# Kernel tuning notes

Hardware: AMD Instinct MI355X
Metric: run time of the kernel (lower is better)

## Reference

```python
import jax, jax.numpy as jnp
import numpy as np

B, S, H = 4, 1024, 1024
NH, HD = 16, 64  # num heads, head dim


def setup_inputs() -> dict:
    key = jax.random.key(0)
    ks = jax.random.split(key, 7)
    scale = 1.0 / np.sqrt(H)
    return {
        "hidden_states": jax.random.normal(ks[0], (B, S, H), jnp.float32),
        "attention_mask": jnp.zeros((B, 1, 1, S), jnp.float32),
        "Wq": jax.random.normal(ks[1], (H, H), jnp.float32) * scale,
        "bq": jnp.zeros((H,), jnp.float32),
        "Wk": jax.random.normal(ks[2], (H, H), jnp.float32) * scale,
        "bk": jnp.zeros((H,), jnp.float32),
        "Wv": jax.random.normal(ks[3], (H, H), jnp.float32) * scale,
        "bv": jnp.zeros((H,), jnp.float32),
    }


def _heads(x):
    # [B,S,H] -> [B,NH,S,HD]
    return x.reshape(x.shape[0], x.shape[1], NH, HD).transpose(0, 2, 1, 3)


def reference(hidden_states, attention_mask, Wq, bq, Wk, bk, Wv, bv):
    q = _heads(hidden_states @ Wq + bq)  # [B,NH,S,HD]
    k = _heads(hidden_states @ Wk + bk)
    v = _heads(hidden_states @ Wv + bv)
    scores = jnp.einsum("bhqd,bhkd->bhqk", q, k) / np.sqrt(HD)
    scores = scores + attention_mask  # broadcast additive mask
    probs = jax.nn.softmax(scores, axis=-1)  # dropout p=0 (eval)
    ctx = jnp.einsum("bhqk,bhkd->bhqd", probs, v)
    # [B,NH,S,HD] -> [B,S,H]
    return ctx.transpose(0, 2, 1, 3).reshape(hidden_states.shape[0], hidden_states.shape[1], NH * HD)
```

## Files before the change

### kernel.cpp

```cpp
#include <hip/hip_runtime.h>
#include <hip/hip_bf16.h>

typedef __bf16 bf16_t;
typedef __bf16 bf16x8 __attribute__((ext_vector_type(8)));
typedef float f32x4 __attribute__((ext_vector_type(4)));
typedef float f32x16 __attribute__((ext_vector_type(16)));
typedef unsigned uint2v __attribute__((ext_vector_type(2)));

#define MFMA16(a, b, c) __builtin_amdgcn_mfma_f32_16x16x32_bf16((a), (b), (c), 0, 0, 0)
#define MFMA32(a, b, c) __builtin_amdgcn_mfma_f32_32x32x16_bf16((a), (b), (c), 0, 0, 0)

static constexpr int BB = 4, SS = 1024, HH = 1024, NHEAD = 16, HDIM = 64;
static constexpr int MM = BB * SS;

__device__ __forceinline__ void gload_lds16(const void* g, void* l) {
  __builtin_amdgcn_global_load_lds((const __attribute__((address_space(1))) void*)g,
                                   (__attribute__((address_space(3))) void*)l, 16, 0, 0);
}

#if __has_builtin(__builtin_amdgcn_permlane32_swap)
#define PSWAP(a, b)                                                    \
  {                                                                    \
    uint2v _r = __builtin_amdgcn_permlane32_swap((a), (b), false, false); \
    (a) = _r.x;                                                        \
    (b) = _r.y;                                                        \
  }
#else
#define PSWAP(a, b) asm("v_permlane32_swap_b32 %0, %1" : "+v"(a), "+v"(b))
#endif

#if __has_builtin(__builtin_amdgcn_exp2f)
__device__ __forceinline__ float EXP2(float x) { return __builtin_amdgcn_exp2f(x); }
#else
__device__ __forceinline__ float EXP2(float x) {
  float r;
  asm("v_exp_f32 %0, %1" : "=v"(r) : "v"(x));
  return r;
}
#endif

__global__ __launch_bounds__(256) void cvt_bf16_kernel(const float* __restrict__ in,
                                                       bf16_t* __restrict__ out, int n) {
  int i = (blockIdx.x * 256 + threadIdx.x) * 8;
  if (i >= n) return;
  float4 a = *(const float4*)(in + i);
  float4 b = *(const float4*)(in + i + 4);
  union { int4 i4; bf16_t h[8]; } u;
  u.h[0] = (bf16_t)a.x; u.h[1] = (bf16_t)a.y; u.h[2] = (bf16_t)a.z; u.h[3] = (bf16_t)a.w;
  u.h[4] = (bf16_t)b.x; u.h[5] = (bf16_t)b.y; u.h[6] = (bf16_t)b.z; u.h[7] = (bf16_t)b.w;
  *(int4*)(out + i) = u.i4;
}

__global__ __launch_bounds__(256) void transposeW_kernel(const float* __restrict__ Wq,
                                                         const float* __restrict__ Wk,
                                                         const float* __restrict__ Wv,
                                                         bf16_t* __restrict__ WT) {
  __shared__ float tile[32][33];
  int z = blockIdx.z;
  const float* W = (z == 0) ? Wq : (z == 1) ? Wk : Wv;
  bf16_t* Out = WT + (size_t)z * HH * HH;
  int tx = threadIdx.x, ty = threadIdx.y;
  int x0 = blockIdx.x * 32;
  int y0 = blockIdx.y * 32;
  for (int j = ty; j < 32; j += 8)
    tile[j][tx] = W[(size_t)(y0 + j) * HH + x0 + tx];
  __syncthreads();
  for (int j = ty; j < 32; j += 8)
    Out[(size_t)(x0 + j) * HH + y0 + tx] = (bf16_t)tile[tx][j];
}

#define BMT 128
#define BNT 384
#define BKT 64
#define NTL 16
#define BUFBYTES 65536

__global__ __launch_bounds__(512, 2) void qkv_gemm2(const bf16_t* __restrict__ hiddenB,
                                                    const bf16_t* __restrict__ WT,
                                                    const float* __restrict__ bq,
                                                    const float* __restrict__ bk,
                                                    const float* __restrict__ bv,
                                                    bf16_t* __restrict__ Qo,
                                                    bf16_t* __restrict__ Ko,
                                                    bf16_t* __restrict__ Vt) {
  __shared__ bf16_t smem[2 * BUFBYTES / 2];

  const int wg = blockIdx.x;
  const int id = (wg & 7) * 32 + (wg >> 3);
  const int nb = id & 7;
  const int mb = id >> 3;

  const int t = threadIdx.x;
  const int lane = t & 63;
  const int w = t >> 6;
  const int wr = w >> 2;
  const int wc = w & 3;
  const int lr = lane & 15;
  const int g4 = lane >> 4;

  const unsigned schunk = (((unsigned)(t & 7)) ^ ((unsigned)((t >> 3) & 7))) << 4;
  const char* Ag = (const char*)hiddenB + (size_t)(mb * BMT) * 2048;
  const char* Bg = (const char*)WT + (size_t)(nb * BNT) * 2048;

  auto stage = [&](const char* gb, int growbase, int kbyte, char* ldsdest) {
    gload_lds16(gb + (size_t)(growbase + (t >> 3)) * 2048 + kbyte + schunk,
                ldsdest + w * 1024);
  };
  const unsigned axor = ((unsigned)(lr & 7)) << 4;

  f32x4 acc[4][6] = {};

  {
    char* S0 = (char*)smem;
    stage(Ag, 0, 0, S0);
    stage(Ag, 64, 0, S0 + 8192);
#pragma unroll
    for (int i = 0; i < 6; ++i) stage(Bg, i * 64, 0, S0 + 16384 + i * 8192);
  }
  asm volatile("s_waitcnt vmcnt(0)" ::: "memory");
  __builtin_amdgcn_s_barrier();

  for (int j = 0; j < NTL; ++j) {
    const char* Ab = (const char*)smem + (j & 1) * BUFBYTES;
    const char* Bb = Ab + 16384;
    char* Sb = (char*)smem + ((j + 1) & 1) * BUFBYTES;
    const int kb = (j + 1) * 128;
    const bool st = (j + 1 < NTL);

    if (st) { stage(Ag, 0, kb, Sb); stage(Ag, 64, kb, Sb + 8192); }

    bf16x8 af[4][2];
#pragma unroll
    for (int mi = 0; mi < 4; ++mi)
#pragma unroll
      for (int ks = 0; ks < 2; ++ks)
        af[mi][ks] = *(const bf16x8*)(Ab + (size_t)(wr * 64 + mi * 16 + lr) * 128 +
                                      (((unsigned)(ks * 64 + g4 * 16)) ^ axor));

#pragma unroll
    for (int p = 0; p < 3; ++p) {
      if (st) {
        stage(Bg, (2 * p) * 64, kb, Sb + 16384 + (2 * p) * 8192);
        stage(Bg, (2 * p + 1) * 64, kb, Sb + 16384 + (2 * p + 1) * 8192);
      }
      bf16x8 b0[2], b1[2];
#pragma unroll
      for (int ks = 0; ks < 2; ++ks) {
        b0[ks] = *(const bf16x8*)(Bb + (size_t)(wc * 96 + (2 * p) * 16 + lr) * 128 +
                                  (((unsigned)(ks * 64 + g4 * 16)) ^ axor));
        b1[ks] = *(const bf16x8*)(Bb + (size_t)(wc * 96 + (2 * p + 1) * 16 + lr) * 128 +
                                  (((unsigned)(ks * 64 + g4 * 16)) ^ axor));
      }
      __builtin_amdgcn_s_setprio(1);
#pragma unroll
      for (int mi = 0; mi < 4; ++mi)
#pragma unroll
        for (int ks = 0; ks < 2; ++ks) {
          acc[mi][2 * p] = MFMA16(af[mi][ks], b0[ks], acc[mi][2 * p]);
          acc[mi][2 * p + 1] = MFMA16(af[mi][ks], b1[ks], acc[mi][2 * p + 1]);
        }
      __builtin_amdgcn_s_setprio(0);
    }

    if (st) {
      asm volatile("s_waitcnt vmcnt(0)" ::: "memory");
      __builtin_amdgcn_s_barrier();
    }
  }

#pragma unroll
  for (int ni = 0; ni < 6; ++ni) {
    int col = nb * BNT + wc * 96 + ni * 16 + lr;
    int z = col >> 10;
    int ci = col & 1023;
    const float* bias = (z == 0) ? bq : (z == 1) ? bk : bv;
    float bia = bias[ci];
    int hh = ci >> 6, d = ci & 63;
    if (z < 2) {
      bf16_t* Out = (z == 0) ? Qo : Ko;
#pragma unroll
      for (int mi = 0; mi < 4; ++mi) {
#pragma unroll
        for (int r = 0; r < 4; ++r) {
          int row = mb * BMT + wr * 64 + mi * 16 + g4 * 4 + r;
          int b = row >> 10, s = row & 1023;
          Out[((size_t)(b * NHEAD + hh) * SS + s) * HDIM + d] = (bf16_t)(acc[mi][ni][r] + bia);
        }
      }
    } else {
#pragma unroll
      for (int mi = 0; mi < 4; ++mi) {
        int row0 = mb * BMT + wr * 64 + mi * 16 + g4 * 4;
        int b = row0 >> 10, s0 = row0 & 1023;
        float v0 = acc[mi][ni][0] + bia, v1 = acc[mi][ni][1] + bia;
        float v2 = acc[mi][ni][2] + bia, v3 = acc[mi][ni][3] + bia;
        unsigned u0, u1;
        asm("v_cvt_pk_bf16_f32 %0, %1, %2" : "=v"(u0) : "v"(v0), "v"(v1));
        asm("v_cvt_pk_bf16_f32 %0, %1, %2" : "=v"(u1) : "v"(v2), "v"(v3));
        uint2 pv; pv.x = u0; pv.y = u1;
        *(uint2*)&Vt[((size_t)(b * NHEAD + hh) * HDIM + d) * SS + s0] = pv;
      }
    }
  }
}

__global__ __launch_bounds__(256) void attn5_kernel(const bf16_t* __restrict__ Q,
                                                    const bf16_t* __restrict__ K,
                                                    const bf16_t* __restrict__ Vt,
                                                    const float* __restrict__ mask,
                                                    float* __restrict__ out) {
  __shared__ bf16_t KVsm[3][2][64 * 64];
  __shared__ float Msm[SS];

  const int wg = blockIdx.x;
  const int id = (wg & 7) * 64 + (wg >> 3);
  const int xblk = id & 7;
  const int bh = id >> 3;

  const int b = bh >> 4;
  const int h = bh & 15;
  const int t = threadIdx.x;
  const int lane = t & 63;
  const int w = t >> 6;
  const int l31 = lane & 31;
  const int hi = lane >> 5;
  const int q0 = xblk * 128 + w * 32;

  const bf16_t* Qh = Q + (size_t)bh * SS * HDIM;
  const bf16_t* Kh = K + (size_t)bh * SS * HDIM;
  const bf16_t* Vh = Vt + (size_t)bh * HDIM * SS;

  const float L2E = 1.4426950408889634f;
  {
    float4 mv = *(const float4*)&mask[(size_t)b * SS + t * 4];
    mv.x *= L2E; mv.y *= L2E; mv.z *= L2E; mv.w *= L2E;
    *(float4*)&Msm[t * 4] = mv;
  }

  bf16x8 qb[4];
#pragma unroll
  for (int c = 0; c < 4; ++c) {
    bf16x8 q = *(const bf16x8*)&Qh[(size_t)(q0 + l31) * HDIM + c * 16 + hi * 8];
#pragma unroll
    for (int e = 0; e < 8; ++e) q[e] = (bf16_t)((float)q[e] * (0.125f * L2E));
    qb[c] = q;
  }

  const int srow = lane >> 3;
  const unsigned gcol = ((lane & 7) * 16) ^ (srow << 4);
  const unsigned swz = (unsigned)((l31 & 7) << 4);

  auto stageKV = [&](int tile, int buf) {
    const int kv0 = tile * 64;
#pragma unroll
    for (int i = 0; i < 2; ++i) {
      int rbase = w * 16 + i * 8;
      gload_lds16((const char*)Kh + (size_t)(kv0 + rbase + srow) * 128 + gcol,
                  (char*)&KVsm[buf][0][0] + (size_t)rbase * 128);
      gload_lds16((const char*)Vh + (size_t)(rbase + srow) * 2048 + (size_t)kv0 * 2 + gcol,
                  (char*)&KVsm[buf][1][0] + (size_t)rbase * 128);
    }
  };

  f32x16 acc0 = {}, acc1 = {};
  float m_run = -1e30f, l_run = 0.f;

  stageKV(0, 0);
  stageKV(1, 1);
  asm volatile("s_waitcnt vmcnt(4) lgkmcnt(0)" ::: "memory");
  __builtin_amdgcn_s_barrier();

  for (int tt = 0; tt < 16; ++tt) {
    if (tt + 2 < 16) stageKV(tt + 2, (tt + 2) % 3);
    const char* Kb = (const char*)&KVsm[tt % 3][0][0];
    const char* Vb = (const char*)&KVsm[tt % 3][1][0];
    const int kv0 = tt * 64;

    f32x16 st0 = {}, st1 = {};
    __builtin_amdgcn_s_setprio(1);
#pragma unroll
    for (int c = 0; c < 4; ++c) {
      bf16x8 kf0 = *(const bf16x8*)(Kb + (size_t)l31 * 128 + ((unsigned)(c * 32 + hi * 16) ^ swz));
      st0 = MFMA32(kf0, qb[c], st0);
    }
#pragma unroll
    for (int c = 0; c < 4; ++c) {
      bf16x8 kf1 = *(const bf16x8*)(Kb + (size_t)(32 + l31) * 128 + ((unsigned)(c * 32 + hi * 16) ^ swz));
      st1 = MFMA32(kf1, qb[c], st1);
    }
    __builtin_amdgcn_s_setprio(0);

#pragma unroll
    for (int k2 = 0; k2 < 8; ++k2) {
      int off = 8 * (k2 >> 1) + 4 * hi + 2 * (k2 & 1);
      float2 m0v = *(const float2*)&Msm[kv0 + off];
      float2 m1v = *(const float2*)&Msm[kv0 + 32 + off];
      st0[2 * k2] += m0v.x; st0[2 * k2 + 1] += m0v.y;
      st1[2 * k2] += m1v.x; st1[2 * k2 + 1] += m1v.y;
    }

    float v0 = fmaxf(st0[0], st1[0]),  v1 = fmaxf(st0[1], st1[1]);
    float v2 = fmaxf(st0[2], st1[2]),  v3 = fmaxf(st0[3], st1[3]);
    float v4 = fmaxf(st0[4], st1[4]),  v5 = fmaxf(st0[5], st1[5]);
    float v6 = fmaxf(st0[6], st1[6]),  v7 = fmaxf(st0[7], st1[7]);
    float v8 = fmaxf(st0[8], st1[8]),  v9 = fmaxf(st0[9], st1[9]);
    float v10 = fmaxf(st0[10], st1[10]), v11 = fmaxf(st0[11], st1[11]);
    float v12 = fmaxf(st0[12], st1[12]), v13 = fmaxf(st0[13], st1[13]);
    float v14 = fmaxf(st0[14], st1[14]), v15 = fmaxf(st0[15], st1[15]);
    float g0 = fmaxf(fmaxf(v0, v1), v2);
    float g1 = fmaxf(fmaxf(v3, v4), v5);
    float g2 = fmaxf(fmaxf(v6, v7), v8);
    float g3 = fmaxf(fmaxf(v9, v10), v11);
    float g4 = fmaxf(fmaxf(v12, v13), v14);
    float mj = fmaxf(fmaxf(fmaxf(g0, g1), g2), fmaxf(fmaxf(g3, g4), v15));
    mj = fmaxf(mj, __shfl_xor(mj, 32));

    if (!__all(mj <= m_run + 8.f)) {
      float mnew = fmaxf(m_run, mj);
      float corr = EXP2(m_run - mnew);
#pragma unroll
      for (int r = 0; r < 16; ++r) { acc0[r] *= corr; acc1[r] *= corr; }
      l_run *= corr;
      m_run = mnew;
    }

#pragma unroll
    for (int r = 0; r < 16; ++r) st0[r] = EXP2(st0[r] - m_run);
#pragma unroll
    for (int r = 0; r < 16; ++r) st1[r] = EXP2(st1[r] - m_run);

    float s0 = (st0[0] + st1[0]) + (st0[1] + st1[1]);
    float s1 = (st0[2] + st1[2]) + (st0[3] + st1[3]);
    float s2 = (st0[4] + st1[4]) + (st0[5] + st1[5]);
    float s3 = (st0[6] + st1[6]) + (st0[7] + st1[7]);
    float s4 = (st0[8] + st1[8]) + (st0[9] + st1[9]);
    float s5 = (st0[10] + st1[10]) + (st0[11] + st1[11]);
    float s6 = (st0[12] + st1[12]) + (st0[13] + st1[13]);
    float s7 = (st0[14] + st1[14]) + (st0[15] + st1[15]);
    float ls = ((s0 + s1) + (s2 + s3)) + ((s4 + s5) + (s6 + s7));
    ls += __shfl_xor(ls, 32);
    l_run += ls;

    unsigned wd0[8], wd1[8];
#pragma unroll
    for (int k2 = 0; k2 < 8; ++k2) {
      unsigned r0, r1;
      float a0f = st0[2 * k2], a1f = st0[2 * k2 + 1];
      float b0f = st1[2 * k2], b1f = st1[2 * k2 + 1];
      asm("v_cvt_pk_bf16_f32 %0, %1, %2" : "=v"(r0) : "v"(a0f), "v"(a1f));
      asm("v_cvt_pk_bf16_f32 %0, %1, %2" : "=v"(r1) : "v"(b0f), "v"(b1f));
      wd0[k2] = r0; wd1[k2] = r1;
    }
    unsigned a0 = wd0[0], b0 = wd0[2]; PSWAP(a0, b0);
    unsigned a1 = wd0[1], b1 = wd0[3]; PSWAP(a1, b1);
    unsigned a2 = wd0[4], b2 = wd0[6]; PSWAP(a2, b2);
    unsigned a3 = wd0[5], b3 = wd0[7]; PSWAP(a3, b3);
    unsigned c0 = wd1[0], d0 = wd1[2]; PSWAP(c0, d0);
    unsigned c1 = wd1[1], d1 = wd1[3]; PSWAP(c1, d1);
    unsigned c2 = wd1[4], d2 = wd1[6]; PSWAP(c2, d2);
    unsigned c3 = wd1[5], d3 = wd1[7]; PSWAP(c3, d3);
    union { unsigned u[4]; bf16x8 v; } pf0, pf1, pf2, pf3;
    pf0.u[0] = a0; pf0.u[1] = a1; pf0.u[2] = b0; pf0.u[3] = b1;
    pf1.u[0] = a2; pf1.u[1] = a3; pf1.u[2] = b2; pf1.u[3] = b3;
    pf2.u[0] = c0; pf2.u[1] = c1; pf2.u[2] = d0; pf2.u[3] = d1;
    pf3.u[0] = c2; pf3.u[1] = c3; pf3.u[2] = d2; pf3.u[3] = d3;

    __builtin_amdgcn_s_setprio(1);
    {
      bf16x8 vf;
      vf = *(const bf16x8*)(Vb + (size_t)(0 * 32 + l31) * 128 + ((unsigned)(0 * 64 + 0 * 32 + hi * 16) ^ swz));
      acc0 = MFMA32(vf, pf0.v, acc0);
      vf = *(const bf16x8*)(Vb + (size_t)(1 * 32 + l31) * 128 + ((unsigned)(0 * 64 + 0 * 32 + hi * 16) ^ swz));
      acc1 = MFMA32(vf, pf0.v, acc1);
      vf = *(const bf16x8*)(Vb + (size_t)(0 * 32 + l31) * 128 + ((unsigned)(0 * 64 + 1 * 32 + hi * 16) ^ swz));
      acc0 = MFMA32(vf, pf1.v, acc0);
      vf = *(const bf16x8*)(Vb + (size_t)(1 * 32 + l31) * 128 + ((unsigned)(0 * 64 + 1 * 32 + hi * 16) ^ swz));
      acc1 = MFMA32(vf, pf1.v, acc1);
      vf = *(const bf16x8*)(Vb + (size_t)(0 * 32 + l31) * 128 + ((unsigned)(1 * 64 + 0 * 32 + hi * 16) ^ swz));
      acc0 = MFMA32(vf, pf2.v, acc0);
      vf = *(const bf16x8*)(Vb + (size_t)(1 * 32 + l31) * 128 + ((unsigned)(1 * 64 + 0 * 32 + hi * 16) ^ swz));
      acc1 = MFMA32(vf, pf2.v, acc1);
      vf = *(const bf16x8*)(Vb + (size_t)(0 * 32 + l31) * 128 + ((unsigned)(1 * 64 + 1 * 32 + hi * 16) ^ swz));
      acc0 = MFMA32(vf, pf3.v, acc0);
      vf = *(const bf16x8*)(Vb + (size_t)(1 * 32 + l31) * 128 + ((unsigned)(1 * 64 + 1 * 32 + hi * 16) ^ swz));
      acc1 = MFMA32(vf, pf3.v, acc1);
    }
    __builtin_amdgcn_s_setprio(0);

    if (tt < 14) {
      asm volatile("s_waitcnt vmcnt(4)" ::: "memory");
      __builtin_amdgcn_s_barrier();
    } else if (tt == 14) {
      asm volatile("s_waitcnt vmcnt(0)" ::: "memory");
      __builtin_amdgcn_s_barrier();
    }
  }

  float rinv = 1.0f / l_run;
  int q = q0 + l31;
  float* ob = out + ((size_t)(b * SS + q)) * HH + h * HDIM;
#pragma unroll
  for (int g = 0; g < 4; ++g) {
    float4 o0, o1;
    o0.x = acc0[g * 4 + 0] * rinv; o0.y = acc0[g * 4 + 1] * rinv;
    o0.z = acc0[g * 4 + 2] * rinv; o0.w = acc0[g * 4 + 3] * rinv;
    o1.x = acc1[g * 4 + 0] * rinv; o1.y = acc1[g * 4 + 1] * rinv;
    o1.z = acc1[g * 4 + 2] * rinv; o1.w = acc1[g * 4 + 3] * rinv;
    *(float4*)&ob[g * 8 + 4 * hi] = o0;
    *(float4*)&ob[32 + g * 8 + 4 * hi] = o1;
  }
}

extern "C" void kernel_launch(void* const* d_in, const int* in_sizes, int n_in,
                              void* d_out, int out_size, void* d_ws, size_t ws_size,
                              hipStream_t stream) {
  const float* hs   = (const float*)d_in[0];
  const float* mask = (const float*)d_in[1];
  const float* Wq   = (const float*)d_in[2];
  const float* bq   = (const float*)d_in[3];
  const float* Wk   = (const float*)d_in[4];
  const float* bk   = (const float*)d_in[5];
  const float* Wv   = (const float*)d_in[6];
  const float* bv   = (const float*)d_in[7];
  float* out = (float*)d_out;

  char* ws = (char*)d_ws;
  bf16_t* hiddenB = (bf16_t*)ws;
  bf16_t* WT      = (bf16_t*)(ws + (size_t)8 * 1024 * 1024);
  bf16_t* Qb      = (bf16_t*)(ws + (size_t)14 * 1024 * 1024);
  bf16_t* Kb      = (bf16_t*)(ws + (size_t)22 * 1024 * 1024);
  bf16_t* Vt      = (bf16_t*)(ws + (size_t)30 * 1024 * 1024);

  cvt_bf16_kernel<<<MM * HH / (256 * 8), 256, 0, stream>>>(hs, hiddenB, MM * HH);
  transposeW_kernel<<<dim3(32, 32, 3), dim3(32, 8), 0, stream>>>(Wq, Wk, Wv, WT);
  qkv_gemm2<<<256, 512, 0, stream>>>(hiddenB, WT, bq, bk, bv, Qb, Kb, Vt);
  attn5_kernel<<<512, 256, 0, stream>>>(Qb, Kb, Vt, mask, out);
}
```

Baseline: 78.70 us.

## Split attention KV range across two wave groups with LDS merge of partial softmax

The attention kernel now launches 512 threads per block. Two groups of four waves each process half of the key/value sequence with double buffering, where before four waves streamed a triple-buffered pipeline over the full sequence. The second half writes its partial accumulators and running max/sum into LDS, and the first half rescales and merges them before writing output. This doubles the waves available to hide latency, but adds a merge step and uses a shallower prefetch with a full vmcnt(0) wait every iteration.

```diff
diff --git a/kernel.cpp b/kernel.cpp
--- a/kernel.cpp
+++ b/kernel.cpp
@@ -29,15 +29,11 @@
 #define PSWAP(a, b) asm("v_permlane32_swap_b32 %0, %1" : "+v"(a), "+v"(b))
 #endif
 
-#if __has_builtin(__builtin_amdgcn_exp2f)
-__device__ __forceinline__ float EXP2(float x) { return __builtin_amdgcn_exp2f(x); }
-#else
 __device__ __forceinline__ float EXP2(float x) {
   float r;
   asm("v_exp_f32 %0, %1" : "=v"(r) : "v"(x));
   return r;
 }
-#endif
 
 __global__ __launch_bounds__(256) void cvt_bf16_kernel(const float* __restrict__ in,
                                                        bf16_t* __restrict__ out, int n) {
@@ -204,12 +200,12 @@
   }
 }
 
-__global__ __launch_bounds__(256) void attn5_kernel(const bf16_t* __restrict__ Q,
-                                                    const bf16_t* __restrict__ K,
-                                                    const bf16_t* __restrict__ Vt,
-                                                    const float* __restrict__ mask,
-                                                    float* __restrict__ out) {
-  __shared__ bf16_t KVsm[3][2][64 * 64];
+__global__ __launch_bounds__(512, 4) void attn6_kernel(const bf16_t* __restrict__ Q,
+                                                       const bf16_t* __restrict__ K,
+                                                       const bf16_t* __restrict__ Vt,
+                                                       const float* __restrict__ mask,
+                                                       float* __restrict__ out) {
+  __shared__ bf16_t KVsm[2][2][2][64 * 64];
   __shared__ float Msm[SS];
 
   const int wg = blockIdx.x;
@@ -222,16 +218,19 @@
   const int t = threadIdx.x;
   const int lane = t & 63;
   const int w = t >> 6;
+  const int wl = w & 3;
+  const int half = w >> 2;
   const int l31 = lane & 31;
   const int hi = lane >> 5;
-  const int q0 = xblk * 128 + w * 32;
+  const int q0 = xblk * 128 + wl * 32;
+  const int kvbase = half * 512;
 
   const bf16_t* Qh = Q + (size_t)bh * SS * HDIM;
   const bf16_t* Kh = K + (size_t)bh * SS * HDIM;
   const bf16_t* Vh = Vt + (size_t)bh * HDIM * SS;
 
   const float L2E = 1.4426950408889634f;
-  {
+  if (t < 256) {
     float4 mv = *(const float4*)&mask[(size_t)b * SS + t * 4];
     mv.x *= L2E; mv.y *= L2E; mv.z *= L2E; mv.w *= L2E;
     *(float4*)&Msm[t * 4] = mv;
@@ -251,14 +250,14 @@
   const unsigned swz = (unsigned)((l31 & 7) << 4);
 
   auto stageKV = [&](int tile, int buf) {
-    const int kv0 = tile * 64;
+    const int kv0 = kvbase + tile * 64;
 #pragma unroll
     for (int i = 0; i < 2; ++i) {
-      int rbase = w * 16 + i * 8;
+      int rbase = wl * 16 + i * 8;
       gload_lds16((const char*)Kh + (size_t)(kv0 + rbase + srow) * 128 + gcol,
-                  (char*)&KVsm[buf][0][0] + (size_t)rbase * 128);
+                  (char*)&KVsm[half][buf][0][0] + (size_t)rbase * 128);
       gload_lds16((const char*)Vh + (size_t)(rbase + srow) * 2048 + (size_t)kv0 * 2 + gcol,
-                  (char*)&KVsm[buf][1][0] + (size_t)rbase * 128);
+                  (char*)&KVsm[half][buf][1][0] + (size_t)rbase * 128);
     }
   };
 
@@ -266,15 +265,14 @@
   float m_run = -1e30f, l_run = 0.f;
 
   stageKV(0, 0);
-  stageKV(1, 1);
-  asm volatile("s_waitcnt vmcnt(4) lgkmcnt(0)" ::: "memory");
+  asm volatile("s_waitcnt vmcnt(0)" ::: "memory");
   __builtin_amdgcn_s_barrier();
 
-  for (int tt = 0; tt < 16; ++tt) {
-    if (tt + 2 < 16) stageKV(tt + 2, (tt + 2) % 3);
-    const char* Kb = (const char*)&KVsm[tt % 3][0][0];
-    const char* Vb = (const char*)&KVsm[tt % 3][1][0];
-    const int kv0 = tt * 64;
+  for (int tt = 0; tt < 8; ++tt) {
+    if (tt + 1 < 8) stageKV(tt + 1, (tt + 1) & 1);
+    const char* Kb = (const char*)&KVsm[half][tt & 1][0][0];
+    const char* Vb = (const char*)&KVsm[half][tt & 1][1][0];
+    const int kv0 = kvbase + tt * 64;
 
     f32x16 st0 = {}, st1 = {};
     __builtin_amdgcn_s_setprio(1);
@@ -368,46 +366,69 @@
     __builtin_amdgcn_s_setprio(1);
     {
       bf16x8 vf;
-      vf = *(const bf16x8*)(Vb + (size_t)(0 * 32 + l31) * 128 + ((unsigned)(0 * 64 + 0 * 32 + hi * 16) ^ swz));
+      vf = *(const bf16x8*)(Vb + (size_t)(l31) * 128 + ((unsigned)(0 * 32 + hi * 16) ^ swz));
       acc0 = MFMA32(vf, pf0.v, acc0);
-      vf = *(const bf16x8*)(Vb + (size_t)(1 * 32 + l31) * 128 + ((unsigned)(0 * 64 + 0 * 32 + hi * 16) ^ swz));
+      vf = *(const bf16x8*)(Vb + (size_t)(32 + l31) * 128 + ((unsigned)(0 * 32 + hi * 16) ^ swz));
       acc1 = MFMA32(vf, pf0.v, acc1);
-      vf = *(const bf16x8*)(Vb + (size_t)(0 * 32 + l31) * 128 + ((unsigned)(0 * 64 + 1 * 32 + hi * 16) ^ swz));
+      vf = *(const bf16x8*)(Vb + (size_t)(l31) * 128 + ((unsigned)(1 * 32 + hi * 16) ^ swz));
       acc0 = MFMA32(vf, pf1.v, acc0);
-      vf = *(const bf16x8*)(Vb + (size_t)(1 * 32 + l31) * 128 + ((unsigned)(0 * 64 + 1 * 32 + hi * 16) ^ swz));
+      vf = *(const bf16x8*)(Vb + (size_t)(32 + l31) * 128 + ((unsigned)(1 * 32 + hi * 16) ^ swz));
       acc1 = MFMA32(vf, pf1.v, acc1);
-      vf = *(const bf16x8*)(Vb + (size_t)(0 * 32 + l31) * 128 + ((unsigned)(1 * 64 + 0 * 32 + hi * 16) ^ swz));
+      vf = *(const bf16x8*)(Vb + (size_t)(l31) * 128 + ((unsigned)(2 * 32 + hi * 16) ^ swz));
       acc0 = MFMA32(vf, pf2.v, acc0);
-      vf = *(const bf16x8*)(Vb + (size_t)(1 * 32 + l31) * 128 + ((unsigned)(1 * 64 + 0 * 32 + hi * 16) ^ swz));
+      vf = *(const bf16x8*)(Vb + (size_t)(32 + l31) * 128 + ((unsigned)(2 * 32 + hi * 16) ^ swz));
       acc1 = MFMA32(vf, pf2.v, acc1);
-      vf = *(const bf16x8*)(Vb + (size_t)(0 * 32 + l31) * 128 + ((unsigned)(1 * 64 + 1 * 32 + hi * 16) ^ swz));
+      vf = *(const bf16x8*)(Vb + (size_t)(l31) * 128 + ((unsigned)(3 * 32 + hi * 16) ^ swz));
       acc0 = MFMA32(vf, pf3.v, acc0);
-      vf = *(const bf16x8*)(Vb + (size_t)(1 * 32 + l31) * 128 + ((unsigned)(1 * 64 + 1 * 32 + hi * 16) ^ swz));
+      vf = *(const bf16x8*)(Vb + (size_t)(32 + l31) * 128 + ((unsigned)(3 * 32 + hi * 16) ^ swz));
       acc1 = MFMA32(vf, pf3.v, acc1);
     }
     __builtin_amdgcn_s_setprio(0);
 
-    if (tt < 14) {
-      asm volatile("s_waitcnt vmcnt(4)" ::: "memory");
-      __builtin_amdgcn_s_barrier();
-    } else if (tt == 14) {
-      asm volatile("s_waitcnt vmcnt(0)" ::: "memory");
-      __builtin_amdgcn_s_barrier();
-    }
-  }
-
-  float rinv = 1.0f / l_run;
-  int q = q0 + l31;
-  float* ob = out + ((size_t)(b * SS + q)) * HH + h * HDIM;
-#pragma unroll
-  for (int g = 0; g < 4; ++g) {
-    float4 o0, o1;
-    o0.x = acc0[g * 4 + 0] * rinv; o0.y = acc0[g * 4 + 1] * rinv;
-    o0.z = acc0[g * 4 + 2] * rinv; o0.w = acc0[g * 4 + 3] * rinv;
-    o1.x = acc1[g * 4 + 0] * rinv; o1.y = acc1[g * 4 + 1] * rinv;
-    o1.z = acc1[g * 4 + 2] * rinv; o1.w = acc1[g * 4 + 3] * rinv;
-    *(float4*)&ob[g * 8 + 4 * hi] = o0;
-    *(float4*)&ob[32 + g * 8 + 4 * hi] = o1;
+    asm volatile("s_waitcnt vmcnt(0)" ::: "memory");
+    __builtin_amdgcn_s_barrier();
+  }
+
+  __syncthreads();
+  float* mb = (float*)&KVsm[0][0][0][0];
+  if (half == 1) {
+    float* dst = mb + ((size_t)(wl * 64 + lane)) * 36;
+#pragma unroll
+    for (int g = 0; g < 4; ++g) {
+      float4 w0, w1;
+      w0.x = acc0[g * 4 + 0]; w0.y = acc0[g * 4 + 1];
+      w0.z = acc0[g * 4 + 2]; w0.w = acc0[g * 4 + 3];
+      w1.x = acc1[g * 4 + 0]; w1.y = acc1[g * 4 + 1];
+      w1.z = acc1[g * 4 + 2]; w1.w = acc1[g * 4 + 3];
+      *(float4*)(dst + g * 4) = w0;
+      *(float4*)(dst + 16 + g * 4) = w1;
+    }
+    dst[32] = m_run; dst[33] = l_run;
+  }
+  __syncthreads();
+  if (half == 0) {
+    const float* src = mb + ((size_t)(wl * 64 + lane)) * 36;
+    float m1 = src[32], l1 = src[33];
+    float m = fmaxf(m_run, m1);
+    float f0 = EXP2(m_run - m), f1 = EXP2(m1 - m);
+    float rinv = 1.0f / (l_run * f0 + l1 * f1);
+    float fr0 = f0 * rinv, fr1 = f1 * rinv;
+    int q = q0 + l31;
+    float* ob = out + ((size_t)(b * SS + q)) * HH + h * HDIM;
+#pragma unroll
+    for (int g = 0; g < 4; ++g) {
+      float4 o0, o1;
+      o0.x = acc0[g * 4 + 0] * fr0 + src[g * 4 + 0] * fr1;
+      o0.y = acc0[g * 4 + 1] * fr0 + src[g * 4 + 1] * fr1;
+      o0.z = acc0[g * 4 + 2] * fr0 + src[g * 4 + 2] * fr1;
+      o0.w = acc0[g * 4 + 3] * fr0 + src[g * 4 + 3] * fr1;
+      o1.x = acc1[g * 4 + 0] * fr0 + src[16 + g * 4 + 0] * fr1;
+      o1.y = acc1[g * 4 + 1] * fr0 + src[16 + g * 4 + 1] * fr1;
+      o1.z = acc1[g * 4 + 2] * fr0 + src[16 + g * 4 + 2] * fr1;
+      o1.w = acc1[g * 4 + 3] * fr0 + src[16 + g * 4 + 3] * fr1;
+      *(float4*)&ob[g * 8 + 4 * hi] = o0;
+      *(float4*)&ob[32 + g * 8 + 4 * hi] = o1;
+    }
   }
 }
 
@@ -434,5 +455,5 @@
   cvt_bf16_kernel<<<MM * HH / (256 * 8), 256, 0, stream>>>(hs, hiddenB, MM * HH);
   transposeW_kernel<<<dim3(32, 32, 3), dim3(32, 8), 0, stream>>>(Wq, Wk, Wv, WT);
   qkv_gemm2<<<256, 512, 0, stream>>>(hiddenB, WT, bq, bk, bv, Qb, Kb, Vt);
-  attn5_kernel<<<512, 256, 0, stream>>>(Qb, Kb, Vt, mask, out);
-}
+  attn6_kernel<<<512, 512, 0, stream>>>(Qb, Kb, Vt, mask, out);
+}
```

After: 75.00 us. -4.7%, faster.
